# Kernel optimization log

Measured on AMD Instinct MI355X. Metric: run time of the kernel, lower is better.

## Reference

```python
import jax, jax.numpy as jnp
import numpy as np

B, S, D, H = 4, 2048, 1024, 16
HD = D // H  # 64


def apply_rotary(x, cos, sin):
    # x: (b, h, s, hd); cos/sin: (s, hd)
    x1, x2 = x[..., : HD // 2], x[..., HD // 2 :]
    rotated = jnp.concatenate((-x2, x1), axis=-1)
    return x * cos + rotated * sin


def setup_inputs() -> dict:
    key = jax.random.key(0)
    ks = jax.random.split(key, 12)
    x = jax.random.normal(ks[0], (B, S, D), dtype=jnp.float32)
    # RoPE tables
    inv_freq = 1.0 / (10000.0 ** (jnp.arange(0, HD, 2, dtype=jnp.float32) / HD))
    t = jnp.arange(S, dtype=jnp.float32)
    freqs = jnp.outer(t, inv_freq)            # (S, HD/2)
    emb = jnp.concatenate((freqs, freqs), -1)  # (S, HD)
    cos, sin = jnp.cos(emb), jnp.sin(emb)
    # causal additive mask
    neg = jnp.finfo(jnp.float32).min
    attn_mask = jnp.where(jnp.tril(jnp.ones((S, S), dtype=bool)), 0.0, neg)[None, None]
    sc = 1.0 / np.sqrt(D)
    Wq = jax.random.normal(ks[1], (D, D), jnp.float32) * sc
    bq = jnp.zeros((D,), jnp.float32)
    Wk = jax.random.normal(ks[2], (D, D), jnp.float32) * sc
    bk = jnp.zeros((D,), jnp.float32)
    Wv = jax.random.normal(ks[3], (D, D), jnp.float32) * sc
    bv = jnp.zeros((D,), jnp.float32)
    Wo = jax.random.normal(ks[4], (D, D), jnp.float32) * sc
    bo = jnp.zeros((D,), jnp.float32)
    return {"x": x, "cos": cos, "sin": sin, "attn_mask": attn_mask,
            "Wq": Wq, "bq": bq, "Wk": Wk, "bk": bk, "Wv": Wv, "bv": bv,
            "Wo": Wo, "bo": bo}


def reference(x, cos, sin, attn_mask, Wq, bq, Wk, bk, Wv, bv, Wo, bo):
    b, s, d = x.shape
    scale = HD ** -0.5
    def proj(W, bias):
        return (x @ W.T + bias).reshape(b, s, H, HD).transpose(0, 2, 1, 3)
    q = apply_rotary(proj(Wq, bq), cos, sin)
    k = apply_rotary(proj(Wk, bk), cos, sin)
    v = proj(Wv, bv)
    scores = jnp.einsum("bhqd,bhkd->bhqk", q, k) * scale + attn_mask
    w = jax.nn.softmax(scores, axis=-1)  # dropout is identity in eval / p=0
    out = jnp.einsum("bhqk,bhkd->bhqd", w, v)
    out = out.transpose(0, 2, 1, 3).reshape(b, s, d)
    return out @ Wo.T + bo
```

## Files before the change

### kernel.cpp

```cpp
#include <hip/hip_runtime.h>

#define Bc 4
#define Sc 2048
#define Dc 1024
#define Hc 16
#define HDc 64
#define Mrows (Bc * Sc)

typedef __bf16 bf16x8 __attribute__((ext_vector_type(8)));
typedef float f32x4 __attribute__((ext_vector_type(4)));

__device__ __forceinline__ unsigned short f2b(float f) {
  unsigned int u = __builtin_bit_cast(unsigned int, f);
  u += 0x7fffu + ((u >> 16) & 1u);
  return (unsigned short)(u >> 16);
}

__device__ __forceinline__ unsigned int pack2(float lo, float hi) {
  return (unsigned int)f2b(lo) | ((unsigned int)f2b(hi) << 16);
}

__device__ __forceinline__ bf16x8 ld8(const unsigned short* p) {
  return __builtin_bit_cast(bf16x8, *(const uint4*)p);
}

__device__ __forceinline__ f32x4 mfma16(bf16x8 a, bf16x8 b, f32x4 c) {
  return __builtin_amdgcn_mfma_f32_16x16x32_bf16(a, b, c, 0, 0, 0);
}

__device__ __forceinline__ void async16(const unsigned short* g, unsigned short* l) {
  __builtin_amdgcn_global_load_lds(
      (const __attribute__((address_space(1))) unsigned int*)g,
      (__attribute__((address_space(3))) unsigned int*)l, 16, 0, 0);
}

__global__ __launch_bounds__(256) void cast_f2b(const float* __restrict__ src,
                                                unsigned short* __restrict__ dst, int n) {
  int i = (blockIdx.x * blockDim.x + threadIdx.x) * 4;
  if (i >= n) return;
  float4 f = *(const float4*)(src + i);
  ushort4 o;
  o.x = f2b(f.x); o.y = f2b(f.y); o.z = f2b(f.z); o.w = f2b(f.w);
  *(ushort4*)(dst + i) = o;
}

__global__ __launch_bounds__(256) void cast_w4(const float* __restrict__ w0,
                                               const float* __restrict__ w1,
                                               const float* __restrict__ w2,
                                               const float* __restrict__ w3,
                                               unsigned short* __restrict__ o0,
                                               unsigned short* __restrict__ o1,
                                               unsigned short* __restrict__ o2,
                                               unsigned short* __restrict__ o3) {
  const int which = blockIdx.x >> 10;
  const float* src = which == 0 ? w0 : which == 1 ? w1 : which == 2 ? w2 : w3;
  unsigned short* dst = which == 0 ? o0 : which == 1 ? o1 : which == 2 ? o2 : o3;
  const int i = ((blockIdx.x & 1023) * 256 + threadIdx.x) * 4;
  float4 f = *(const float4*)(src + i);
  ushort4 o;
  o.x = f2b(f.x); o.y = f2b(f.y); o.z = f2b(f.z); o.w = f2b(f.w);
  *(ushort4*)(dst + i) = o;
}

__global__ __launch_bounds__(256) void gemm_qkv(const unsigned short* __restrict__ A,
                                                const unsigned short* __restrict__ Wqp,
                                                const unsigned short* __restrict__ Wkp,
                                                const unsigned short* __restrict__ Wvp,
                                                const float* __restrict__ bqp,
                                                const float* __restrict__ bkp,
                                                const float* __restrict__ bvp,
                                                unsigned short* __restrict__ Qo,
                                                unsigned short* __restrict__ Ko,
                                                unsigned short* __restrict__ Vto,
                                                const float* __restrict__ cosT,
                                                const float* __restrict__ sinT) {
  constexpr int K = Dc;
  __shared__ __align__(16) unsigned short As[128 * 64];
  __shared__ __align__(16) unsigned short Bs[128 * 64];

  const int which = blockIdx.x >> 3;
  const int nb = (blockIdx.x & 7) * 128;
  const unsigned short* W = which == 0 ? Wqp : which == 1 ? Wkp : Wvp;
  const float* bias = which == 0 ? bqp : which == 1 ? bkp : bvp;
  const int mb = blockIdx.y * 128;
  const int t = threadIdx.x;
  const int lane = t & 63;
  const int quad = lane >> 4, l16 = lane & 15;
  const int wm = (t >> 6) >> 1, wn = (t >> 6) & 1;

  f32x4 acc[4][4] = {};

  const int srow = t >> 3;
  const int schunk = (t & 7) ^ (srow & 7);
  const unsigned short* gA = A + (size_t)(mb + srow) * K + schunk * 8;
  const unsigned short* gW = W + (size_t)(nb + srow) * K + schunk * 8;
  const int ldsOff = t * 8;

  for (int k0 = 0; k0 < K; k0 += 64) {
    __syncthreads();
#pragma unroll
    for (int o = 0; o < 4; ++o) {
      async16(gA + (size_t)o * 32 * K + k0, &As[ldsOff + o * 2048]);
      async16(gW + (size_t)o * 32 * K + k0, &Bs[ldsOff + o * 2048]);
    }
    __syncthreads();

#pragma unroll
    for (int kk = 0; kk < 2; ++kk) {
      bf16x8 af[4], bf[4];
#pragma unroll
      for (int i = 0; i < 4; ++i) {
        const int ar = wm * 64 + i * 16 + l16;
        af[i] = ld8(&As[ar * 64 + ((kk * 4 + quad) ^ (ar & 7)) * 8]);
        const int br = wn * 64 + i * 16 + l16;
        bf[i] = ld8(&Bs[br * 64 + ((kk * 4 + quad) ^ (br & 7)) * 8]);
      }
#pragma unroll
      for (int i = 0; i < 4; ++i)
#pragma unroll
        for (int j = 0; j < 4; ++j)
          acc[i][j] = mfma16(af[i], bf[j], acc[i][j]);
    }
  }

  float bn[4];
#pragma unroll
  for (int j = 0; j < 4; ++j) bn[j] = bias[nb + wn * 64 + j * 16 + l16];

  if (which < 2) {
    unsigned short* out = which == 0 ? Qo : Ko;
    const float sc = which == 0 ? 0.125f : 1.0f;
#pragma unroll
    for (int i = 0; i < 4; ++i)
#pragma unroll
      for (int r = 0; r < 4; ++r) {
        const int m = mb + wm * 64 + i * 16 + quad * 4 + r;
        const int s = m & (Sc - 1);
        float v[4];
#pragma unroll
        for (int j = 0; j < 4; ++j) v[j] = acc[i][j][r] + bn[j];
#pragma unroll
        for (int j = 0; j < 4; ++j) {
          const int hd = j * 16 + l16;
          const float c = cosT[s * HDc + hd];
          const float sn = sinT[s * HDc + hd];
          float o = (j < 2) ? (v[j] * c - v[j ^ 2] * sn)
                            : (v[j] * c + v[j ^ 2] * sn);
          out[(size_t)m * Dc + nb + wn * 64 + hd] = f2b(o * sc);
        }
      }
  } else {
#pragma unroll
    for (int i = 0; i < 4; ++i)
#pragma unroll
      for (int r = 0; r < 4; ++r) {
        const int m = mb + wm * 64 + i * 16 + quad * 4 + r;
        const int s = m & (Sc - 1);
        const int b = m >> 11;
#pragma unroll
        for (int j = 0; j < 4; ++j) {
          const int n = nb + wn * 64 + j * 16 + l16;
          const int h = n >> 6, hd = n & 63;
          Vto[(size_t)((b * Hc + h) * HDc + hd) * Sc + s] = f2b(acc[i][j][r] + bn[j]);
        }
      }
  }
}

__global__ __launch_bounds__(256) void gemm_out(const unsigned short* __restrict__ A,
                                                const unsigned short* __restrict__ W,
                                                const float* __restrict__ bias,
                                                float* __restrict__ out) {
  constexpr int N = Dc, K = Dc;
  __shared__ __align__(16) unsigned short As[128 * 64];
  __shared__ __align__(16) unsigned short Bs[128 * 64];

  const int nb = blockIdx.x * 128;
  const int mb = blockIdx.y * 128;
  const int t = threadIdx.x;
  const int lane = t & 63;
  const int quad = lane >> 4, l16 = lane & 15;
  const int wm = (t >> 6) >> 1, wn = (t >> 6) & 1;

  f32x4 acc[4][4] = {};

  const int srow = t >> 3;
  const int schunk = (t & 7) ^ (srow & 7);
  const unsigned short* gA = A + (size_t)(mb + srow) * K + schunk * 8;
  const unsigned short* gW = W + (size_t)(nb + srow) * K + schunk * 8;
  const int ldsOff = t * 8;

  for (int k0 = 0; k0 < K; k0 += 64) {
    __syncthreads();
#pragma unroll
    for (int o = 0; o < 4; ++o) {
      async16(gA + (size_t)o * 32 * K + k0, &As[ldsOff + o * 2048]);
      async16(gW + (size_t)o * 32 * K + k0, &Bs[ldsOff + o * 2048]);
    }
    __syncthreads();

#pragma unroll
    for (int kk = 0; kk < 2; ++kk) {
      bf16x8 af[4], bf[4];
#pragma unroll
      for (int i = 0; i < 4; ++i) {
        const int ar = wm * 64 + i * 16 + l16;
        af[i] = ld8(&As[ar * 64 + ((kk * 4 + quad) ^ (ar & 7)) * 8]);
        const int br = wn * 64 + i * 16 + l16;
        bf[i] = ld8(&Bs[br * 64 + ((kk * 4 + quad) ^ (br & 7)) * 8]);
      }
#pragma unroll
      for (int i = 0; i < 4; ++i)
#pragma unroll
        for (int j = 0; j < 4; ++j)
          acc[i][j] = mfma16(af[i], bf[j], acc[i][j]);
    }
  }

  float bn[4];
#pragma unroll
  for (int j = 0; j < 4; ++j) bn[j] = bias[nb + wn * 64 + j * 16 + l16];
#pragma unroll
  for (int i = 0; i < 4; ++i)
#pragma unroll
    for (int r = 0; r < 4; ++r) {
      const int m = mb + wm * 64 + i * 16 + quad * 4 + r;
#pragma unroll
      for (int j = 0; j < 4; ++j)
        out[(size_t)m * N + nb + wn * 64 + j * 16 + l16] = acc[i][j][r] + bn[j];
    }
}

#define FIXMAX 16.0f
__global__ __launch_bounds__(256) void attn_kernel(const unsigned short* __restrict__ Q,
                                                   const unsigned short* __restrict__ K,
                                                   const unsigned short* __restrict__ Vt,
                                                   unsigned short* __restrict__ O) {
  __shared__ __align__(16) unsigned short Ks[2][64 * 64];
  __shared__ __align__(16) unsigned short Vs[2][64 * 64];

  const int bh = blockIdx.x;
  const int qt = (gridDim.y - 1) - blockIdx.y;
  const int b = bh >> 4, h = bh & 15;
  const int wave = threadIdx.x >> 6, lane = threadIdx.x & 63;
  const int quad = lane >> 4, l16 = lane & 15;
  const int qbase = qt * 128;
  const int wbase = qbase + wave * 32;
  const int wave_max_q = wbase + 31;
  const int nkt = 2 * qt + 2;

  int kSrc[2], vSrc[2], sDst[2];
#pragma unroll
  for (int o = 0; o < 2; ++o) {
    const int R = wave * 16 + o * 8 + (lane >> 3);
    const int slot = lane & 7;
    const int rr = R & 31;
    const int key = (R >> 5) * 32 + ((rr >> 2) & 3) * 8 + ((rr >> 4) & 1) * 4 + (rr & 3);
    const int chunk = slot ^ (R & 7);
    kSrc[o] = key * Dc + chunk * 8;
    vSrc[o] = R * Sc + chunk * 8;
    sDst[o] = wave * 1024 + o * 512 + lane * 8;
  }
  const unsigned short* kBase = K + (size_t)b * Sc * Dc + h * HDc;
  const unsigned short* vBase = Vt + (size_t)(b * Hc + h) * HDc * Sc;

  auto stage = [&](int buf, int kb) {
#pragma unroll
    for (int o = 0; o < 2; ++o) {
      async16(kBase + (size_t)kb * Dc + kSrc[o], &Ks[buf][sDst[o]]);
      async16(vBase + kb + vSrc[o], &Vs[buf][sDst[o]]);
    }
  };

  bf16x8 qf[2][2];
#pragma unroll
  for (int mt = 0; mt < 2; ++mt) {
    const unsigned short* qp =
        Q + (size_t)(b * Sc + wbase + mt * 16 + l16) * Dc + h * HDc + quad * 8;
    qf[mt][0] = ld8(qp);
    qf[mt][1] = ld8(qp + 32);
  }

  float lsum[2] = {0.f, 0.f};
  f32x4 accO[2][4] = {};

  stage(0, 0);
  for (int t = 0; t < nkt; ++t) {
    __syncthreads();
    if (t + 1 < nkt) stage((t + 1) & 1, (t + 1) * 64);
    const int kb = t * 64;
    if (kb > wave_max_q) continue;
    const unsigned short* KsB = &Ks[t & 1][0];
    const unsigned short* VsB = &Vs[t & 1][0];

#pragma unroll
    for (int c = 0; c < 2; ++c) {
      const int kc = kb + c * 32;
      if (kc > wave_max_q) break;
      const bool partial = (kc + 31 > wbase);

      bf16x8 kf[2][2], vf[4];
#pragma unroll
      for (int tt = 0; tt < 2; ++tt) {
        const int row = c * 32 + tt * 16 + l16;
#pragma unroll
        for (int kk = 0; kk < 2; ++kk)
          kf[tt][kk] = ld8(&KsB[row * 64 + (((kk * 4 + quad) ^ (l16 & 7)) * 8)]);
      }
#pragma unroll
      for (int ct = 0; ct < 4; ++ct)
        vf[ct] = ld8(&VsB[(ct * 16 + l16) * 64 + (((c * 4 + quad) ^ (l16 & 7)) * 8)]);

#pragma unroll
      for (int mt = 0; mt < 2; ++mt) {
        f32x4 st[2];
#pragma unroll
        for (int tt = 0; tt < 2; ++tt) {
          st[tt] = mfma16(kf[tt][0], qf[mt][0], f32x4{0.f, 0.f, 0.f, 0.f});
          st[tt] = mfma16(kf[tt][1], qf[mt][1], st[tt]);
        }
        const int q = wbase + mt * 16 + l16;
        unsigned int w[4];
        float ls = 0.f;
#pragma unroll
        for (int tt = 0; tt < 2; ++tt)
#pragma unroll
          for (int rp = 0; rp < 2; ++rp) {
            const int key0 = kc + quad * 8 + tt * 4 + 2 * rp;
            float s0 = st[tt][2 * rp], s1 = st[tt][2 * rp + 1];
            if (partial) {
              s0 = (key0     <= q) ? s0 : -1e30f;
              s1 = (key0 + 1 <= q) ? s1 : -1e30f;
            }
            const float p0 = __expf(s0 - FIXMAX);
            const float p1 = __expf(s1 - FIXMAX);
            ls += p0 + p1;
            w[tt * 2 + rp] = pack2(p0, p1);
          }
        lsum[mt] += ls;
        const bf16x8 pB = __builtin_bit_cast(bf16x8, uint4{w[0], w[1], w[2], w[3]});
#pragma unroll
        for (int ct = 0; ct < 4; ++ct)
          accO[mt][ct] = mfma16(vf[ct], pB, accO[mt][ct]);
      }
    }
  }

#pragma unroll
  for (int mt = 0; mt < 2; ++mt) {
    float l = lsum[mt];
    l += __shfl_xor(l, 16);
    l += __shfl_xor(l, 32);
    const float inv = 1.f / l;
    const int m = wbase + mt * 16 + l16;
    unsigned short* op = O + (size_t)(b * Sc + m) * Dc + h * HDc;
#pragma unroll
    for (int ct = 0; ct < 4; ++ct) {
      const unsigned int lo = pack2(accO[mt][ct][0] * inv, accO[mt][ct][1] * inv);
      const unsigned int hi = pack2(accO[mt][ct][2] * inv, accO[mt][ct][3] * inv);
      *(uint2*)(op + ct * 16 + quad * 4) = uint2{lo, hi};
    }
  }
}

extern "C" void kernel_launch(void* const* d_in, const int* in_sizes, int n_in,
                              void* d_out, int out_size, void* d_ws, size_t ws_size,
                              hipStream_t stream) {
  const float* x = (const float*)d_in[0];
  const float* cosT = (const float*)d_in[1];
  const float* sinT = (const float*)d_in[2];
  const float* Wq = (const float*)d_in[4];
  const float* bq = (const float*)d_in[5];
  const float* Wk = (const float*)d_in[6];
  const float* bk = (const float*)d_in[7];
  const float* Wv = (const float*)d_in[8];
  const float* bv = (const float*)d_in[9];
  const float* Wo = (const float*)d_in[10];
  const float* bo = (const float*)d_in[11];

  char* p = (char*)d_ws;
  auto alloc = [&](size_t bytes) { char* r = p; p += bytes; return r; };
  const size_t XB = (size_t)Mrows * Dc * 2;
  const size_t WB = (size_t)Dc * Dc * 2;
  unsigned short* xb  = (unsigned short*)alloc(XB);
  unsigned short* wqb = (unsigned short*)alloc(WB);
  unsigned short* wkb = (unsigned short*)alloc(WB);
  unsigned short* wvb = (unsigned short*)alloc(WB);
  unsigned short* wob = (unsigned short*)alloc(WB);
  unsigned short* Qb  = (unsigned short*)alloc(XB);
  unsigned short* Kb  = (unsigned short*)alloc(XB);
  unsigned short* Vtb = (unsigned short*)alloc(XB);
  unsigned short* Ob  = (unsigned short*)alloc(XB);

  const int nX = Mrows * Dc;
  cast_f2b<<<nX / 1024, 256, 0, stream>>>(x, xb, nX);
  cast_w4<<<4096, 256, 0, stream>>>(Wq, Wk, Wv, Wo, wqb, wkb, wvb, wob);

  gemm_qkv<<<dim3(24, Mrows / 128), 256, 0, stream>>>(
      xb, wqb, wkb, wvb, bq, bk, bv, Qb, Kb, Vtb, cosT, sinT);

  attn_kernel<<<dim3(Bc * Hc, Sc / 128), 256, 0, stream>>>(Qb, Kb, Vtb, Ob);

  gemm_out<<<dim3(Dc / 128, Mrows / 128), 256, 0, stream>>>(Ob, wob, bo, (float*)d_out);
}
```

Measured before the change: 278.5 us.

## Pair causal query tiles per block, use exp2 softmax, truncating pack, merged casts

The attention grid is halved so that each block processes a short and a long causal query tile (qt and 15-qt), balancing work across blocks. The softmax now uses exp2, with log2(e) folded into the Q scale and the fixed max offset preloaded into the MFMA accumulator. Probabilities are packed to bf16 by truncation through a byte permute. The two cast kernels are merged into one launch. Truncation adds a small bias to the bf16 probabilities, and a fixed max still risks overflow if scores are large.

Result: faster. 270.5 us (-2.9%).

```diff
diff --git a/kernel.cpp b/kernel.cpp
--- a/kernel.cpp
+++ b/kernel.cpp
@@ -10,6 +10,9 @@
 typedef __bf16 bf16x8 __attribute__((ext_vector_type(8)));
 typedef float f32x4 __attribute__((ext_vector_type(4)));
 
+#define FIX2 23.0831207f
+#define QSCALE 0.18033688f
+
 __device__ __forceinline__ unsigned short f2b(float f) {
   unsigned int u = __builtin_bit_cast(unsigned int, f);
   u += 0x7fffu + ((u >> 16) & 1u);
@@ -20,6 +23,19 @@
   return (unsigned int)f2b(lo) | ((unsigned int)f2b(hi) << 16);
 }
 
+__device__ __forceinline__ unsigned int pack2t(float lo, float hi) {
+  return __builtin_amdgcn_perm(__builtin_bit_cast(unsigned int, hi),
+                               __builtin_bit_cast(unsigned int, lo), 0x07060302u);
+}
+
+__device__ __forceinline__ float fexp2(float x) {
+#if __has_builtin(__builtin_amdgcn_exp2f)
+  return __builtin_amdgcn_exp2f(x);
+#else
+  return exp2f(x);
+#endif
+}
+
 __device__ __forceinline__ bf16x8 ld8(const unsigned short* p) {
   return __builtin_bit_cast(bf16x8, *(const uint4*)p);
 }
@@ -34,28 +50,28 @@
       (__attribute__((address_space(3))) unsigned int*)l, 16, 0, 0);
 }
 
-__global__ __launch_bounds__(256) void cast_f2b(const float* __restrict__ src,
-                                                unsigned short* __restrict__ dst, int n) {
-  int i = (blockIdx.x * blockDim.x + threadIdx.x) * 4;
-  if (i >= n) return;
-  float4 f = *(const float4*)(src + i);
-  ushort4 o;
-  o.x = f2b(f.x); o.y = f2b(f.y); o.z = f2b(f.z); o.w = f2b(f.w);
-  *(ushort4*)(dst + i) = o;
-}
-
-__global__ __launch_bounds__(256) void cast_w4(const float* __restrict__ w0,
-                                               const float* __restrict__ w1,
-                                               const float* __restrict__ w2,
-                                               const float* __restrict__ w3,
-                                               unsigned short* __restrict__ o0,
-                                               unsigned short* __restrict__ o1,
-                                               unsigned short* __restrict__ o2,
-                                               unsigned short* __restrict__ o3) {
-  const int which = blockIdx.x >> 10;
-  const float* src = which == 0 ? w0 : which == 1 ? w1 : which == 2 ? w2 : w3;
-  unsigned short* dst = which == 0 ? o0 : which == 1 ? o1 : which == 2 ? o2 : o3;
-  const int i = ((blockIdx.x & 1023) * 256 + threadIdx.x) * 4;
+__global__ __launch_bounds__(256) void cast_all(const float* __restrict__ x,
+                                                const float* __restrict__ w0,
+                                                const float* __restrict__ w1,
+                                                const float* __restrict__ w2,
+                                                const float* __restrict__ w3,
+                                                unsigned short* __restrict__ xo,
+                                                unsigned short* __restrict__ o0,
+                                                unsigned short* __restrict__ o1,
+                                                unsigned short* __restrict__ o2,
+                                                unsigned short* __restrict__ o3) {
+  int blk = blockIdx.x;
+  const float* src;
+  unsigned short* dst;
+  if (blk < 8192) {
+    src = x; dst = xo;
+  } else {
+    const int which = (blk - 8192) >> 10;
+    src = which == 0 ? w0 : which == 1 ? w1 : which == 2 ? w2 : w3;
+    dst = which == 0 ? o0 : which == 1 ? o1 : which == 2 ? o2 : o3;
+    blk = (blk - 8192) & 1023;
+  }
+  const int i = (blk * 256 + threadIdx.x) * 4;
   float4 f = *(const float4*)(src + i);
   ushort4 o;
   o.x = f2b(f.x); o.y = f2b(f.y); o.z = f2b(f.z); o.w = f2b(f.w);
@@ -129,7 +145,7 @@
 
   if (which < 2) {
     unsigned short* out = which == 0 ? Qo : Ko;
-    const float sc = which == 0 ? 0.125f : 1.0f;
+    const float sc = which == 0 ? QSCALE : 1.0f;
 #pragma unroll
     for (int i = 0; i < 4; ++i)
 #pragma unroll
@@ -231,7 +247,6 @@
     }
 }
 
-#define FIXMAX 16.0f
 __global__ __launch_bounds__(256) void attn_kernel(const unsigned short* __restrict__ Q,
                                                    const unsigned short* __restrict__ K,
                                                    const unsigned short* __restrict__ Vt,
@@ -240,14 +255,9 @@
   __shared__ __align__(16) unsigned short Vs[2][64 * 64];
 
   const int bh = blockIdx.x;
-  const int qt = (gridDim.y - 1) - blockIdx.y;
   const int b = bh >> 4, h = bh & 15;
   const int wave = threadIdx.x >> 6, lane = threadIdx.x & 63;
   const int quad = lane >> 4, l16 = lane & 15;
-  const int qbase = qt * 128;
-  const int wbase = qbase + wave * 32;
-  const int wave_max_q = wbase + 31;
-  const int nkt = 2 * qt + 2;
 
   int kSrc[2], vSrc[2], sDst[2];
 #pragma unroll
@@ -272,93 +282,103 @@
     }
   };
 
-  bf16x8 qf[2][2];
-#pragma unroll
-  for (int mt = 0; mt < 2; ++mt) {
-    const unsigned short* qp =
-        Q + (size_t)(b * Sc + wbase + mt * 16 + l16) * Dc + h * HDc + quad * 8;
-    qf[mt][0] = ld8(qp);
-    qf[mt][1] = ld8(qp + 32);
-  }
-
-  float lsum[2] = {0.f, 0.f};
-  f32x4 accO[2][4] = {};
-
-  stage(0, 0);
-  for (int t = 0; t < nkt; ++t) {
+#pragma unroll 1
+  for (int sidx = 0; sidx < 2; ++sidx) {
+    const int qt = sidx == 0 ? (int)blockIdx.y : 15 - (int)blockIdx.y;
+    const int qbase = qt * 128;
+    const int wbase = qbase + wave * 32;
+    const int wave_max_q = wbase + 31;
+    const int nkt = 2 * qt + 2;
+
+    bf16x8 qf[2][2];
+#pragma unroll
+    for (int mt = 0; mt < 2; ++mt) {
+      const unsigned short* qp =
+          Q + (size_t)(b * Sc + wbase + mt * 16 + l16) * Dc + h * HDc + quad * 8;
+      qf[mt][0] = ld8(qp);
+      qf[mt][1] = ld8(qp + 32);
+    }
+
+    float lsum[2] = {0.f, 0.f};
+    f32x4 accO[2][4] = {};
+
     __syncthreads();
-    if (t + 1 < nkt) stage((t + 1) & 1, (t + 1) * 64);
-    const int kb = t * 64;
-    if (kb > wave_max_q) continue;
-    const unsigned short* KsB = &Ks[t & 1][0];
-    const unsigned short* VsB = &Vs[t & 1][0];
-
-#pragma unroll
-    for (int c = 0; c < 2; ++c) {
-      const int kc = kb + c * 32;
-      if (kc > wave_max_q) break;
-      const bool partial = (kc + 31 > wbase);
-
-      bf16x8 kf[2][2], vf[4];
-#pragma unroll
-      for (int tt = 0; tt < 2; ++tt) {
-        const int row = c * 32 + tt * 16 + l16;
-#pragma unroll
-        for (int kk = 0; kk < 2; ++kk)
-          kf[tt][kk] = ld8(&KsB[row * 64 + (((kk * 4 + quad) ^ (l16 & 7)) * 8)]);
-      }
-#pragma unroll
-      for (int ct = 0; ct < 4; ++ct)
-        vf[ct] = ld8(&VsB[(ct * 16 + l16) * 64 + (((c * 4 + quad) ^ (l16 & 7)) * 8)]);
-
-#pragma unroll
-      for (int mt = 0; mt < 2; ++mt) {
-        f32x4 st[2];
+    stage(0, 0);
+    for (int t = 0; t < nkt; ++t) {
+      __syncthreads();
+      if (t + 1 < nkt) stage((t + 1) & 1, (t + 1) * 64);
+      const int kb = t * 64;
+      if (kb > wave_max_q) continue;
+      const unsigned short* KsB = &Ks[t & 1][0];
+      const unsigned short* VsB = &Vs[t & 1][0];
+
+#pragma unroll
+      for (int c = 0; c < 2; ++c) {
+        const int kc = kb + c * 32;
+        if (kc > wave_max_q) break;
+        const bool partial = (kc + 31 > wbase);
+
+        bf16x8 kf[2][2], vf[4];
 #pragma unroll
         for (int tt = 0; tt < 2; ++tt) {
-          st[tt] = mfma16(kf[tt][0], qf[mt][0], f32x4{0.f, 0.f, 0.f, 0.f});
-          st[tt] = mfma16(kf[tt][1], qf[mt][1], st[tt]);
+          const int row = c * 32 + tt * 16 + l16;
+#pragma unroll
+          for (int kk = 0; kk < 2; ++kk)
+            kf[tt][kk] = ld8(&KsB[row * 64 + (((kk * 4 + quad) ^ (l16 & 7)) * 8)]);
         }
-        const int q = wbase + mt * 16 + l16;
-        unsigned int w[4];
-        float ls = 0.f;
-#pragma unroll
-        for (int tt = 0; tt < 2; ++tt)
-#pragma unroll
-          for (int rp = 0; rp < 2; ++rp) {
-            const int key0 = kc + quad * 8 + tt * 4 + 2 * rp;
-            float s0 = st[tt][2 * rp], s1 = st[tt][2 * rp + 1];
-            if (partial) {
-              s0 = (key0     <= q) ? s0 : -1e30f;
-              s1 = (key0 + 1 <= q) ? s1 : -1e30f;
+#pragma unroll
+        for (int ct = 0; ct < 4; ++ct)
+          vf[ct] = ld8(&VsB[(ct * 16 + l16) * 64 + (((c * 4 + quad) ^ (l16 & 7)) * 8)]);
+
+#pragma unroll
+        for (int mt = 0; mt < 2; ++mt) {
+          f32x4 st[2];
+#pragma unroll
+          for (int tt = 0; tt < 2; ++tt) {
+            st[tt] = mfma16(kf[tt][0], qf[mt][0], f32x4{-FIX2, -FIX2, -FIX2, -FIX2});
+            st[tt] = mfma16(kf[tt][1], qf[mt][1], st[tt]);
+          }
+          const int q = wbase + mt * 16 + l16;
+          unsigned int w[4];
+          float ls = 0.f;
+#pragma unroll
+          for (int tt = 0; tt < 2; ++tt)
+#pragma unroll
+            for (int rp = 0; rp < 2; ++rp) {
+              const int key0 = kc + quad * 8 + tt * 4 + 2 * rp;
+              float s0 = st[tt][2 * rp], s1 = st[tt][2 * rp + 1];
+              if (partial) {
+                s0 = (key0     <= q) ? s0 : -1e30f;
+                s1 = (key0 + 1 <= q) ? s1 : -1e30f;
+              }
+              const float p0 = fexp2(s0);
+              const float p1 = fexp2(s1);
+              ls += p0 + p1;
+              w[tt * 2 + rp] = pack2t(p0, p1);
             }
-            const float p0 = __expf(s0 - FIXMAX);
-            const float p1 = __expf(s1 - FIXMAX);
-            ls += p0 + p1;
-            w[tt * 2 + rp] = pack2(p0, p1);
-          }
-        lsum[mt] += ls;
-        const bf16x8 pB = __builtin_bit_cast(bf16x8, uint4{w[0], w[1], w[2], w[3]});
-#pragma unroll
-        for (int ct = 0; ct < 4; ++ct)
-          accO[mt][ct] = mfma16(vf[ct], pB, accO[mt][ct]);
-      }
-    }
-  }
-
-#pragma unroll
-  for (int mt = 0; mt < 2; ++mt) {
-    float l = lsum[mt];
-    l += __shfl_xor(l, 16);
-    l += __shfl_xor(l, 32);
-    const float inv = 1.f / l;
-    const int m = wbase + mt * 16 + l16;
-    unsigned short* op = O + (size_t)(b * Sc + m) * Dc + h * HDc;
-#pragma unroll
-    for (int ct = 0; ct < 4; ++ct) {
-      const unsigned int lo = pack2(accO[mt][ct][0] * inv, accO[mt][ct][1] * inv);
-      const unsigned int hi = pack2(accO[mt][ct][2] * inv, accO[mt][ct][3] * inv);
-      *(uint2*)(op + ct * 16 + quad * 4) = uint2{lo, hi};
+          lsum[mt] += ls;
+          const bf16x8 pB = __builtin_bit_cast(bf16x8, uint4{w[0], w[1], w[2], w[3]});
+#pragma unroll
+          for (int ct = 0; ct < 4; ++ct)
+            accO[mt][ct] = mfma16(vf[ct], pB, accO[mt][ct]);
+        }
+      }
+    }
+
+#pragma unroll
+    for (int mt = 0; mt < 2; ++mt) {
+      float l = lsum[mt];
+      l += __shfl_xor(l, 16);
+      l += __shfl_xor(l, 32);
+      const float inv = 1.f / l;
+      const int m = wbase + mt * 16 + l16;
+      unsigned short* op = O + (size_t)(b * Sc + m) * Dc + h * HDc;
+#pragma unroll
+      for (int ct = 0; ct < 4; ++ct) {
+        const unsigned int lo = pack2(accO[mt][ct][0] * inv, accO[mt][ct][1] * inv);
+        const unsigned int hi = pack2(accO[mt][ct][2] * inv, accO[mt][ct][3] * inv);
+        *(uint2*)(op + ct * 16 + quad * 4) = uint2{lo, hi};
+      }
     }
   }
 }
@@ -392,14 +412,12 @@
   unsigned short* Vtb = (unsigned short*)alloc(XB);
   unsigned short* Ob  = (unsigned short*)alloc(XB);
 
-  const int nX = Mrows * Dc;
-  cast_f2b<<<nX / 1024, 256, 0, stream>>>(x, xb, nX);
-  cast_w4<<<4096, 256, 0, stream>>>(Wq, Wk, Wv, Wo, wqb, wkb, wvb, wob);
+  cast_all<<<12288, 256, 0, stream>>>(x, Wq, Wk, Wv, Wo, xb, wqb, wkb, wvb, wob);
 
   gemm_qkv<<<dim3(24, Mrows / 128), 256, 0, stream>>>(
       xb, wqb, wkb, wvb, bq, bk, bv, Qb, Kb, Vtb, cosT, sinT);
 
-  attn_kernel<<<dim3(Bc * Hc, Sc / 128), 256, 0, stream>>>(Qb, Kb, Vtb, Ob);
+  attn_kernel<<<dim3(Bc * Hc, 8), 256, 0, stream>>>(Qb, Kb, Vtb, Ob);
 
   gemm_out<<<dim3(Dc / 128, Mrows / 128), 256, 0, stream>>>(Ob, wob, bo, (float*)d_out);
 }
```
